# Kernel optimization log

Measured on AMD Instinct MI355X. Metric: run time of the kernel, lower is better.

## Reference

```python
import jax, jax.numpy as jnp
import numpy as np

N_EMBDS = 1024
N_HEADS = 16
HEAD_DIM = N_EMBDS // N_HEADS


def setup_inputs() -> dict:
    key = jax.random.key(0)
    ks = jax.random.split(key, 5)
    B, T, C = 2, 2048, N_EMBDS
    x = jax.random.normal(ks[0], (B, T, C), dtype=jnp.float32)
    s = 1.0 / np.sqrt(C)
    W_attn = jax.random.normal(ks[1], (C, 3 * C), dtype=jnp.float32) * s
    b_attn = jnp.zeros((3 * C,), dtype=jnp.float32)
    W_proj = jax.random.normal(ks[2], (C, C), dtype=jnp.float32) * s
    b_proj = jnp.zeros((C,), dtype=jnp.float32)
    return {"x": x, "W_attn": W_attn, "b_attn": b_attn, "W_proj": W_proj, "b_proj": b_proj}


def reference(x, W_attn, b_attn, W_proj, b_proj):
    B, T, C = x.shape
    H, D = N_HEADS, HEAD_DIM
    qkv = x @ W_attn + b_attn  # [B, T, 3C]
    q, k, v = jnp.split(qkv, 3, axis=-1)
    # [B, H, T, D]
    q = q.reshape(B, T, H, D).transpose(0, 2, 1, 3)
    k = k.reshape(B, T, H, D).transpose(0, 2, 1, 3)
    v = v.reshape(B, T, H, D).transpose(0, 2, 1, 3)
    att = jnp.einsum('bhqd,bhkd->bhqk', q, k) * (1.0 / np.sqrt(D))  # [B,H,T,T]
    causal = jnp.tril(jnp.ones((T, T), dtype=bool))
    att = jnp.where(causal[None, None], att, -jnp.inf)
    att = jax.nn.softmax(att, axis=-1)
    y = jnp.einsum('bhqk,bhkd->bhqd', att, v)  # [B,H,T,D]
    y = y.transpose(0, 2, 1, 3).reshape(B, T, C)
    return y @ W_proj + b_proj
```

## Files before the change

kernel.cpp:

```cpp
#include <hip/hip_runtime.h>
#include <hip/hip_bf16.h>


typedef __bf16 bf16x8 __attribute__((ext_vector_type(8)));
typedef float  f32x4  __attribute__((ext_vector_type(4)));
#define BF16 __hip_bfloat16

constexpr int Bb = 2, Tt = 2048, Cc = 1024, Hh = 16, Dd = 64;
constexpr float NEG_INF = -1e30f;

__device__ __forceinline__ f32x4 mfma16(bf16x8 a, bf16x8 b, f32x4 c) {
  return __builtin_amdgcn_mfma_f32_16x16x32_bf16(a, b, c, 0, 0, 0);
}

__device__ __forceinline__ void gll16(const void* g, void* l) {
  __builtin_amdgcn_global_load_lds((const __attribute__((address_space(1))) void*)g,
                                   (__attribute__((address_space(3))) void*)l,
                                   16, 0, 0);
}

__device__ __forceinline__ int swz64(int r, int c) {
  return r * 64 + ((((c >> 3) ^ r) & 7) << 3) + (c & 7);
}

__device__ __forceinline__ int kperm(int kr) {
  return (((kr >> 5) << 1) + ((kr >> 2) & 1)) * 16 + (((kr >> 3) & 3) << 2) + (kr & 3);
}

__global__ void prep_kernel(const float* __restrict__ x, BF16* __restrict__ xb,
                            const float* __restrict__ Wa, BF16* __restrict__ WaT,
                            const float* __restrict__ Wp, BF16* __restrict__ WpT) {
  __shared__ float tile[32][33];
  const int bx = blockIdx.x, tid = threadIdx.x;
  if (bx < 2048) {
    const int i = (bx * 256 + tid) * 8;
    const float4 a = *(const float4*)&x[i];
    const float4 b = *(const float4*)&x[i + 4];
    BF16 o[8];
    o[0] = __float2bfloat16(a.x); o[1] = __float2bfloat16(a.y);
    o[2] = __float2bfloat16(a.z); o[3] = __float2bfloat16(a.w);
    o[4] = __float2bfloat16(b.x); o[5] = __float2bfloat16(b.y);
    o[6] = __float2bfloat16(b.z); o[7] = __float2bfloat16(b.w);
    *(uint4*)&xb[i] = *(const uint4*)o;
    return;
  }
  const float* in; BF16* outT; int K, N, gx, gy;
  if (bx < 5120) {
    const int idx = bx - 2048;
    in = Wa; outT = WaT; K = 1024; N = 3072; gx = idx % 96; gy = idx / 96;
  } else {
    const int idx = bx - 5120;
    in = Wp; outT = WpT; K = 1024; N = 1024; gx = idx % 32; gy = idx / 32;
  }
  const int n0 = gx * 32, k0 = gy * 32;
  const int tx = tid & 31, ty = tid >> 5;
#pragma unroll
  for (int i = ty; i < 32; i += 8) tile[i][tx] = in[(size_t)(k0 + i) * N + (n0 + tx)];
  __syncthreads();
#pragma unroll
  for (int i = ty; i < 32; i += 8)
    outT[(size_t)(n0 + i) * K + (k0 + tx)] = __float2bfloat16(tile[tx][i]);
}

template <int MODE>
__global__ __launch_bounds__(256) void gemm_bt(const BF16* __restrict__ A,
                                               const BF16* __restrict__ Bt,
                                               const float* __restrict__ bias,
                                               BF16* __restrict__ oq,
                                               BF16* __restrict__ ok,
                                               BF16* __restrict__ ov,
                                               float* __restrict__ fout,
                                               int Ndim, int Kdim) {
  __shared__ alignas(16) BF16 sA[128 * 64];
  __shared__ alignas(16) BF16 sB[128 * 64];
  const int tid = threadIdx.x;
  const int wave = tid >> 6, lane = tid & 63;
  const int quad = lane >> 4, l16 = lane & 15;
  const int wm = (wave >> 1) * 64, wn = (wave & 1) * 64;
  const int bm = blockIdx.y * 128, bn = blockIdx.x * 128;
  const int sw = l16 & 7;

  f32x4 acc[4][4];
#pragma unroll
  for (int i = 0; i < 4; ++i)
#pragma unroll
    for (int j = 0; j < 4; ++j) acc[i][j] = f32x4{0.f, 0.f, 0.f, 0.f};

  const int srow = wave * 32 + (lane >> 3);
  const int sgl = (lane ^ (lane >> 3)) & 7;
  const BF16* gA0 = &A[(size_t)(bm + srow) * Kdim + sgl * 8];
  const BF16* gB0 = &Bt[(size_t)(bn + srow) * Kdim + sgl * 8];
  const size_t rstep8 = (size_t)8 * Kdim;

  for (int k0 = 0; k0 < Kdim; k0 += 64) {
    __syncthreads();
#pragma unroll
    for (int s = 0; s < 4; ++s) {
      gll16(gA0 + s * rstep8 + k0, &sA[wave * 2048 + s * 512]);
      gll16(gB0 + s * rstep8 + k0, &sB[wave * 2048 + s * 512]);
    }
    __syncthreads();

#pragma unroll
    for (int h = 0; h < 2; ++h) {
      bf16x8 af[4], bf_[4];
#pragma unroll
      for (int i = 0; i < 4; ++i)
        af[i] = *(const bf16x8*)
            &sA[(wm + i * 16 + l16) * 64 + (((h * 4 + quad) ^ sw) << 3)];
#pragma unroll
      for (int j = 0; j < 4; ++j)
        bf_[j] = *(const bf16x8*)
            &sB[(wn + j * 16 + l16) * 64 + (((h * 4 + quad) ^ sw) << 3)];
#pragma unroll
      for (int i = 0; i < 4; ++i)
#pragma unroll
        for (int j = 0; j < 4; ++j) acc[i][j] = mfma16(af[i], bf_[j], acc[i][j]);
    }
  }

#pragma unroll
  for (int j = 0; j < 4; ++j) {
    const int gn = bn + wn + j * 16 + l16;
    const float bsv = bias[gn];
    if (MODE == 1) {
#pragma unroll
      for (int i = 0; i < 4; ++i)
#pragma unroll
        for (int r = 0; r < 4; ++r) {
          const int gm = bm + wm + i * 16 + quad * 4 + r;
          fout[(size_t)gm * Ndim + gn] = acc[i][j][r] + bsv;
        }
    } else {
      const int which = (bn + wn + j * 16) >> 10;
      const int c = gn & 1023;
      const int hh = c >> 6, dd = c & 63;
#pragma unroll
      for (int i = 0; i < 4; ++i) {
        const int gm0 = bm + wm + i * 16 + quad * 4;
        const int bb = gm0 >> 11, tk0 = gm0 & 2047;
        const size_t bh = (size_t)(bb * Hh + hh);
        if (which == 2) {
          BF16 tmp[4];
#pragma unroll
          for (int r = 0; r < 4; ++r) tmp[r] = __float2bfloat16(acc[i][j][r] + bsv);
          *(uint2*)&ov[(bh * Dd + dd) * Tt + tk0] = *(const uint2*)tmp;
        } else {
          BF16* dst = (which == 0) ? oq : ok;
          const float scale = (which == 0) ? 0.125f : 1.0f;
#pragma unroll
          for (int r = 0; r < 4; ++r)
            dst[(bh * Tt + tk0 + r) * Dd + dd] =
                __float2bfloat16((acc[i][j][r] + bsv) * scale);
        }
      }
    }
  }
}

__global__ __launch_bounds__(256) void attn_kernel(const BF16* __restrict__ qg,
                                                   const BF16* __restrict__ kg,
                                                   const BF16* __restrict__ vtg,
                                                   BF16* __restrict__ yb) {
  __shared__ alignas(16) BF16 sK[2 * 64 * 64];
  __shared__ alignas(16) BF16 sV[2 * 64 * 64];
  const int id = blockIdx.x;
  const int swz = ((id & 7) << 7) + (id >> 3);
  const int pr = swz & 31, h = (swz >> 5) & 15, b = swz >> 9;
  const int tid = threadIdx.x;
  const int wave = tid >> 6, lane = tid & 63;
  const int quad = lane >> 4, l16 = lane & 15;
  const int qs = (wave >> 1) ? (63 - pr) : pr;
  const int sub = wave & 1;
  const int jt_diag = qs >> 1;
  const int jt_max = (63 - pr) >> 1;
  const size_t base = ((size_t)(b * Hh + h)) * Tt * Dd;
  const int qrow0 = qs * 32 + sub * 16;

  bf16x8 qf0, qf1;
  {
    const size_t off = base + (size_t)(qrow0 + l16) * Dd;
    qf0 = *(const bf16x8*)&qg[off + quad * 8];
    qf1 = *(const bf16x8*)&qg[off + 32 + quad * 8];
  }

  bf16x8 ones8;
#pragma unroll
  for (int j = 0; j < 8; ++j) ones8[j] = (__bf16)1.0f;

  f32x4 o[4], oL;
#pragma unroll
  for (int i = 0; i < 4; ++i) o[i] = f32x4{0.f, 0.f, 0.f, 0.f};
  oL = f32x4{0.f, 0.f, 0.f, 0.f};

  const int krow = tid >> 2, kcg = (tid & 3) * 16;
  const int kprow = kperm(krow);
  const int wK0 = swz64(kprow, kcg), wK1 = swz64(kprow, kcg + 8);
  const int wV0 = swz64(krow, kcg), wV1 = swz64(krow, kcg + 8);

  uint4 rk0, rk1, rv0, rv1;
  {
    const uint4* pk = (const uint4*)&kg[base + (size_t)krow * Dd + kcg];
    const uint4* pv = (const uint4*)&vtg[base + (size_t)krow * Tt + kcg];
    rk0 = pk[0]; rk1 = pk[1];
    rv0 = pv[0]; rv1 = pv[1];
  }

  for (int jt = 0; jt <= jt_max; ++jt) {
    BF16* sKb = &sK[(jt & 1) * 4096];
    BF16* sVb = &sV[(jt & 1) * 4096];
    *(uint4*)&sKb[wK0] = rk0;
    *(uint4*)&sKb[wK1] = rk1;
    *(uint4*)&sVb[wV0] = rv0;
    *(uint4*)&sVb[wV1] = rv1;
    if (jt < jt_max) {
      const int kb2 = (jt + 1) * 64;
      const uint4* nk = (const uint4*)&kg[base + (size_t)(kb2 + krow) * Dd + kcg];
      const uint4* nv = (const uint4*)&vtg[base + (size_t)krow * Tt + kb2 + kcg];
      rk0 = nk[0]; rk1 = nk[1];
      rv0 = nv[0]; rv1 = nv[1];
    }
    __syncthreads();

    if (jt > jt_diag) continue;
    const int kb = jt * 64;

    f32x4 sS[4];
    __builtin_amdgcn_s_setprio(1);
#pragma unroll
    for (int t = 0; t < 4; ++t) {
      const bf16x8 kf0 = *(const bf16x8*)&sKb[swz64(t * 16 + l16, quad * 8)];
      const bf16x8 kf1 = *(const bf16x8*)&sKb[swz64(t * 16 + l16, 32 + quad * 8)];
      sS[t] = mfma16(kf0, qf0, f32x4{0.f, 0.f, 0.f, 0.f});
      sS[t] = mfma16(kf1, qf1, sS[t]);
    }
    __builtin_amdgcn_s_setprio(0);

    if (jt == jt_diag) {
      const int q = qrow0 + l16;
#pragma unroll
      for (int t = 0; t < 4; ++t) {
        const int kc0 = kb + (t >> 1) * 32 + quad * 8 + (t & 1) * 4;
#pragma unroll
        for (int r = 0; r < 4; ++r)
          if (kc0 + r > q) sS[t][r] = NEG_INF;
      }
    }

    bf16x8 pf[2];
#pragma unroll
    for (int cc = 0; cc < 2; ++cc)
#pragma unroll
      for (int j = 0; j < 8; ++j)
        pf[cc][j] = (__bf16)__expf(sS[cc * 2 + (j >> 2)][j & 3] - 12.0f);

    __builtin_amdgcn_s_setprio(1);
#pragma unroll
    for (int cc = 0; cc < 2; ++cc) {
#pragma unroll
      for (int dt = 0; dt < 4; ++dt) {
        const bf16x8 vb =
            *(const bf16x8*)&sVb[swz64(dt * 16 + l16, cc * 32 + quad * 8)];
        o[dt] = mfma16(pf[cc], vb, o[dt]);
      }
      oL = mfma16(pf[cc], ones8, oL);
    }
    __builtin_amdgcn_s_setprio(0);
  }

#pragma unroll
  for (int r = 0; r < 4; ++r) {
    const float inv = 1.0f / oL[r];
    const int trow = qrow0 + quad * 4 + r;
#pragma unroll
    for (int dt = 0; dt < 4; ++dt)
      yb[((size_t)(b * Tt + trow)) * Cc + h * Dd + dt * 16 + l16] =
          __float2bfloat16(o[dt][r] * inv);
  }
}

extern "C" void kernel_launch(void* const* d_in, const int* in_sizes, int n_in,
                              void* d_out, int out_size, void* d_ws, size_t ws_size,
                              hipStream_t stream) {
  (void)in_sizes; (void)n_in; (void)out_size; (void)ws_size;
  const float* x      = (const float*)d_in[0];
  const float* W_attn = (const float*)d_in[1];
  const float* b_attn = (const float*)d_in[2];
  const float* W_proj = (const float*)d_in[3];
  const float* b_proj = (const float*)d_in[4];
  float* out = (float*)d_out;

  constexpr size_t SZ_WA = (size_t)3072 * 1024;
  constexpr size_t SZ_WP = (size_t)1024 * 1024;
  constexpr size_t SZ_X  = (size_t)4096 * 1024;
  constexpr size_t SZ_T  = (size_t)Bb * Hh * Tt * Dd;

  BF16* ws   = (BF16*)d_ws;
  BF16* wtAb = ws;
  BF16* wtPb = wtAb + SZ_WA;
  BF16* xb   = wtPb + SZ_WP;
  BF16* q    = xb + SZ_X;
  BF16* k    = q + SZ_T;
  BF16* vt   = k + SZ_T;
  BF16* yb   = vt + SZ_T;

  prep_kernel<<<dim3(6144), 256, 0, stream>>>(x, xb, W_attn, wtAb, W_proj, wtPb);
  gemm_bt<0><<<dim3(24, 32), 256, 0, stream>>>(xb, wtAb, b_attn, q, k, vt, nullptr,
                                               3072, 1024);
  attn_kernel<<<dim3(1024), 256, 0, stream>>>(q, k, vt, yb);
  gemm_bt<1><<<dim3(8, 32), 256, 0, stream>>>(yb, wtPb, b_proj, nullptr, nullptr,
                                              nullptr, out, 1024, 1024);
}
```

Measured before the change: 182.2 us.

## Load K/V tiles with direct global-to-LDS loads and remap causal attention blocks

```diff
diff --git a/kernel.cpp b/kernel.cpp
--- a/kernel.cpp
+++ b/kernel.cpp
@@ -8,6 +8,8 @@
 
 constexpr int Bb = 2, Tt = 2048, Cc = 1024, Hh = 16, Dd = 64;
 constexpr float NEG_INF = -1e30f;
+constexpr float Q_SCALE = 0.18033688011112042f;
+constexpr float EXP2_BIAS = 17.312340490667562f;
 
 __device__ __forceinline__ f32x4 mfma16(bf16x8 a, bf16x8 b, f32x4 c) {
   return __builtin_amdgcn_mfma_f32_16x16x32_bf16(a, b, c, 0, 0, 0);
@@ -23,8 +25,8 @@
   return r * 64 + ((((c >> 3) ^ r) & 7) << 3) + (c & 7);
 }
 
-__device__ __forceinline__ int kperm(int kr) {
-  return (((kr >> 5) << 1) + ((kr >> 2) & 1)) * 16 + (((kr >> 3) & 3) << 2) + (kr & 3);
+__device__ __forceinline__ int kperm_inv(int r) {
+  return (r & 0x23) | ((r & 0x0C) << 1) | ((r & 0x10) >> 2);
 }
 
 __global__ void prep_kernel(const float* __restrict__ x, BF16* __restrict__ xb,
@@ -147,7 +149,7 @@
           *(uint2*)&ov[(bh * Dd + dd) * Tt + tk0] = *(const uint2*)tmp;
         } else {
           BF16* dst = (which == 0) ? oq : ok;
-          const float scale = (which == 0) ? 0.125f : 1.0f;
+          const float scale = (which == 0) ? Q_SCALE : 1.0f;
 #pragma unroll
           for (int r = 0; r < 4; ++r)
             dst[(bh * Tt + tk0 + r) * Dd + dd] =
@@ -165,17 +167,15 @@
   __shared__ alignas(16) BF16 sK[2 * 64 * 64];
   __shared__ alignas(16) BF16 sV[2 * 64 * 64];
   const int id = blockIdx.x;
-  const int swz = ((id & 7) << 7) + (id >> 3);
-  const int pr = swz & 31, h = (swz >> 5) & 15, b = swz >> 9;
+  const int xcd = id & 7, local = id >> 3;
+  const int bh = xcd * 4 + (local & 3);
+  const int s = 31 - (local >> 2);
+  const int b = bh >> 4, h = bh & 15;
   const int tid = threadIdx.x;
   const int wave = tid >> 6, lane = tid & 63;
   const int quad = lane >> 4, l16 = lane & 15;
-  const int qs = (wave >> 1) ? (63 - pr) : pr;
-  const int sub = wave & 1;
-  const int jt_diag = qs >> 1;
-  const int jt_max = (63 - pr) >> 1;
   const size_t base = ((size_t)(b * Hh + h)) * Tt * Dd;
-  const int qrow0 = qs * 32 + sub * 16;
+  const int qrow0 = s * 64 + wave * 16;
 
   bf16x8 qf0, qf1;
   {
@@ -193,36 +193,34 @@
   for (int i = 0; i < 4; ++i) o[i] = f32x4{0.f, 0.f, 0.f, 0.f};
   oL = f32x4{0.f, 0.f, 0.f, 0.f};
 
-  const int krow = tid >> 2, kcg = (tid & 3) * 16;
-  const int kprow = kperm(krow);
-  const int wK0 = swz64(kprow, kcg), wK1 = swz64(kprow, kcg + 8);
-  const int wV0 = swz64(krow, kcg), wV1 = swz64(krow, kcg + 8);
-
-  uint4 rk0, rk1, rv0, rv1;
-  {
-    const uint4* pk = (const uint4*)&kg[base + (size_t)krow * Dd + kcg];
-    const uint4* pv = (const uint4*)&vtg[base + (size_t)krow * Tt + kcg];
-    rk0 = pk[0]; rk1 = pk[1];
-    rv0 = pv[0]; rv1 = pv[1];
-  }
-
-  for (int jt = 0; jt <= jt_max; ++jt) {
-    BF16* sKb = &sK[(jt & 1) * 4096];
-    BF16* sVb = &sV[(jt & 1) * 4096];
-    *(uint4*)&sKb[wK0] = rk0;
-    *(uint4*)&sKb[wK1] = rk1;
-    *(uint4*)&sVb[wV0] = rv0;
-    *(uint4*)&sVb[wV1] = rv1;
-    if (jt < jt_max) {
-      const int kb2 = (jt + 1) * 64;
-      const uint4* nk = (const uint4*)&kg[base + (size_t)(kb2 + krow) * Dd + kcg];
-      const uint4* nv = (const uint4*)&vtg[base + (size_t)krow * Tt + kb2 + kcg];
-      rk0 = nk[0]; rk1 = nk[1];
-      rv0 = nv[0]; rv1 = nv[1];
-    }
-    __syncthreads();
-
-    if (jt > jt_diag) continue;
+  const int lr = lane >> 3;
+  const int swg = (lane ^ (lane >> 3)) & 7;
+  const int r0 = wave * 16 + lr, r1 = r0 + 8;
+  const BF16* pk0 = &kg[base + (size_t)kperm_inv(r0) * Dd + swg * 8];
+  const BF16* pk1 = &kg[base + (size_t)kperm_inv(r1) * Dd + swg * 8];
+  const BF16* pv0 = &vtg[base + (size_t)r0 * Tt + swg * 8];
+  const BF16* pv1 = &vtg[base + (size_t)r1 * Tt + swg * 8];
+  const int dst0 = wave * 1024, dst1 = dst0 + 512;
+
+  gll16(pk0, &sK[dst0]);
+  gll16(pk1, &sK[dst1]);
+  gll16(pv0, &sV[dst0]);
+  gll16(pv1, &sV[dst1]);
+
+  for (int jt = 0; jt <= s; ++jt) {
+    asm volatile("s_waitcnt vmcnt(0)" ::: "memory");
+    __builtin_amdgcn_s_barrier();
+    const BF16* sKb = &sK[(jt & 1) * 4096];
+    const BF16* sVb = &sV[(jt & 1) * 4096];
+    if (jt < s) {
+      const int nb = ((jt + 1) & 1) * 4096;
+      const size_t ko = (size_t)(jt + 1) * 4096;
+      const int vo = (jt + 1) * 64;
+      gll16(pk0 + ko, &sK[nb + dst0]);
+      gll16(pk1 + ko, &sK[nb + dst1]);
+      gll16(pv0 + vo, &sV[nb + dst0]);
+      gll16(pv1 + vo, &sV[nb + dst1]);
+    }
     const int kb = jt * 64;
 
     f32x4 sS[4];
@@ -236,7 +234,7 @@
     }
     __builtin_amdgcn_s_setprio(0);
 
-    if (jt == jt_diag) {
+    if (jt == s) {
       const int q = qrow0 + l16;
 #pragma unroll
       for (int t = 0; t < 4; ++t) {
@@ -252,7 +250,7 @@
     for (int cc = 0; cc < 2; ++cc)
 #pragma unroll
       for (int j = 0; j < 8; ++j)
-        pf[cc][j] = (__bf16)__expf(sS[cc * 2 + (j >> 2)][j & 3] - 12.0f);
+        pf[cc][j] = (__bf16)exp2f(sS[cc * 2 + (j >> 2)][j & 3] - EXP2_BIAS);
 
     __builtin_amdgcn_s_setprio(1);
 #pragma unroll
```

Result: no change. 183.8 us (+0.9%).
